# Kernel tuning notes

Hardware: AMD Instinct MI355X
Metric: run time of the kernel (lower is better)

Reference implementation:

```python
import jax, jax.numpy as jnp
import numpy as np

DIM = 1024
STEPS = 4
LEAK = 0.9
RESET = 0.0
EPS = 1e-6


def setup_inputs() -> dict:
    key = jax.random.key(0)
    ks = jax.random.split(key, 5)
    sc = 1.0 / np.sqrt(DIM)
    return {
        "x": jax.random.normal(ks[0], (4, 4096, DIM), dtype=jnp.float32),
        "W_in": jax.random.normal(ks[1], (DIM, DIM), dtype=jnp.float32) * sc,
        "W_inh": jax.random.normal(ks[2], (DIM, DIM), dtype=jnp.float32) * sc,
        "W_out": jax.random.normal(ks[3], (DIM, DIM), dtype=jnp.float32) * sc,
        "threshold_vec": jnp.full((DIM,), 0.5, dtype=jnp.float32),
        "norm_weight": jnp.ones((DIM,), dtype=jnp.float32),
    }


def _rmsnorm(y, w):
    # RMSNorm: y * rsqrt(mean(y^2)) * w
    ms = jnp.mean(y * y, axis=-1, keepdims=True)
    return y * jax.lax.rsqrt(ms + EPS) * w


def reference(x, W_in, W_inh, W_out, threshold_vec, norm_weight):
    # x: [B, L, D]
    membrane = jnp.zeros_like(x)
    current = x @ W_in.T  # same every step; computed once (identical math)
    spike_sum = jnp.zeros_like(x)
    prev_spike = None
    for step in range(STEPS):
        membrane = membrane + current
        if step > 0:
            membrane = membrane - 0.1 * (prev_spike @ W_inh.T)
        fire_mask = (membrane > threshold_vec).astype(x.dtype)
        fire_soft = jax.nn.sigmoid((membrane - threshold_vec) * 10.0)
        # straight-through estimator: hard mask fwd, sigmoid grad
        fire_mask_grad = fire_mask - jax.lax.stop_gradient(fire_soft) + fire_soft
        spike = fire_mask_grad * membrane
        spike_sum = spike_sum + spike
        prev_spike = spike
        membrane = (membrane * (1.0 - fire_mask) + RESET * fire_mask) * LEAK
    spike_total = spike_sum / float(STEPS)
    lif_out = spike_total @ W_out.T
    fired_any = (jnp.abs(spike_total) > 1e-6).astype(x.dtype)
    y = x * (1.0 - 0.5 * fired_any) + 0.5 * lif_out
    x_lif = _rmsnorm(y, norm_weight)
    return x_lif, spike_total, membrane
```

## Files before the change

### kernel.cpp

```cpp
#include <hip/hip_runtime.h>
#include <cmath>

#define N_ROWS 16384
#define DIM 1024
#define MARGIN 5e-5
#define MAX_EVENTS 4194304
#define BATCH 8


__global__ __launch_bounds__(64) void zero_cnt(int* cnt) {
  if (threadIdx.x == 0 && blockIdx.x == 0) cnt[0] = 0;
}

__device__ inline void record_event(int* cnt, int* ev, int r, int s, int c) {
  int idx = atomicAdd(cnt, 1);
  if (idx < MAX_EVENTS) ev[idx] = (r << 12) | (s << 10) | c;
}

template<typename TA, int STEP, bool WRITE_SPK>
__global__ __launch_bounds__(256) void gemm_lif(
    const TA* __restrict__ A, const float* __restrict__ B,
    double* __restrict__ cur, double* __restrict__ mem,
    double* __restrict__ spk_out, float* __restrict__ ssum,
    const float* __restrict__ thr, int* cnt, int* ev)
{
  __shared__ double As[16][130];
  __shared__ double Bs[16][130];
  const int tid  = threadIdx.x;
  const int tx   = tid & 15;
  const int ty   = tid >> 4;
  const int col0 = blockIdx.x * 128;
  const int row0 = blockIdx.y * 128;

  const int ar  = tid >> 1;
  const int akc = (tid & 1) * 8;

  double acc[8][8] = {};

  for (int k0 = 0; k0 < DIM; k0 += 16) {
    const TA* ap = &A[(size_t)(row0 + ar) * DIM + (size_t)(k0 + akc)];
#pragma unroll
    for (int u = 0; u < 8; ++u) As[akc + u][ar] = (double)ap[u];
    const float* bp = &B[(size_t)(col0 + ar) * DIM + (size_t)(k0 + akc)];
#pragma unroll
    for (int u = 0; u < 8; ++u) Bs[akc + u][ar] = (double)bp[u];
    __syncthreads();
#pragma unroll
    for (int kk = 0; kk < 16; ++kk) {
      double a[8], b[8];
#pragma unroll
      for (int u = 0; u < 4; ++u) {
        const double2 av = *reinterpret_cast<const double2*>(&As[kk][ty * 8 + 2 * u]);
        a[2 * u] = av.x; a[2 * u + 1] = av.y;
        const double2 bv = *reinterpret_cast<const double2*>(&Bs[kk][tx * 2 + 32 * u]);
        b[2 * u] = bv.x; b[2 * u + 1] = bv.y;
      }
#pragma unroll
      for (int i = 0; i < 8; ++i)
#pragma unroll
        for (int j = 0; j < 8; ++j)
          acc[i][j] = fma(a[i], b[j], acc[i][j]);
    }
    __syncthreads();
  }

#pragma unroll
  for (int i = 0; i < 8; ++i)
#pragma unroll
    for (int j = 0; j < 8; ++j) {
      const int r = row0 + ty * 8 + i;
      const int c = col0 + tx * 2 + (j & 1) + (j >> 1) * 32;
      const size_t e = (size_t)r * DIM + c;
      double m;
      if (STEP == 0) {
        m = acc[i][j];
        cur[e] = m;
      } else {
        const double m1 = __dadd_rn(mem[e], cur[e]);
        const double t2 = __dmul_rn(0.1, acc[i][j]);
        m = __dsub_rn(m1, t2);
      }
      const double t = (double)thr[c];
      if (fabs(m - t) < MARGIN) record_event(cnt, ev, r, STEP, c);
      const bool fire = m > t;
      const double s = fire ? m : 0.0;
      if (WRITE_SPK) spk_out[e] = s;
      if (STEP == 0) ssum[e] = (float)s;
      else           ssum[e] += (float)s;
      mem[e] = fire ? 0.0 : __dmul_rn(m, 0.9);
    }
}

__global__ __launch_bounds__(256) void init_mid(
    const double* __restrict__ mem, const float* __restrict__ ssum,
    float* __restrict__ memlo, float* __restrict__ memhi,
    float* __restrict__ out1)
{
  size_t base = (size_t)blockIdx.x * 2048 + threadIdx.x;
#pragma unroll
  for (int v = 0; v < 8; ++v) {
    size_t e = base + (size_t)v * 256;
    float f = (float)mem[e];
    memlo[e] = f;
    memhi[e] = f;
    out1[e]  = __fmul_rn(ssum[e], 0.25f);
  }
}

__device__ inline void atomicMinF(float* p, float v) {
  unsigned* u = (unsigned*)p;
  unsigned old = __float_as_uint(*p);
  while (__uint_as_float(old) > v) {
    unsigned assumed = old;
    old = atomicCAS(u, assumed, __float_as_uint(v));
    if (old == assumed) break;
  }
}
__device__ inline void atomicMaxF(float* p, float v) {
  unsigned* u = (unsigned*)p;
  unsigned old = __float_as_uint(*p);
  while (__uint_as_float(old) < v) {
    unsigned assumed = old;
    old = atomicCAS(u, assumed, __float_as_uint(v));
    if (old == assumed) break;
  }
}

__global__ __launch_bounds__(256) void transpose_w(
    const float* __restrict__ W, float* __restrict__ Wt)
{
  __shared__ float t[32][33];
  const int bx = blockIdx.x & 31, by = blockIdx.x >> 5;
  const int x = threadIdx.x & 31, y0 = (threadIdx.x >> 5) << 2;
#pragma unroll
  for (int u = 0; u < 4; ++u)
    t[y0 + u][x] = W[(size_t)(by * 32 + y0 + u) * DIM + bx * 32 + x];
  __syncthreads();
#pragma unroll
  for (int u = 0; u < 4; ++u)
    Wt[(size_t)(bx * 32 + y0 + u) * DIM + by * 32 + x] = t[x][y0 + u];
}

__global__ __launch_bounds__(1024) void phase2f(
    const double* __restrict__ cur, const float* __restrict__ Wt,
    const float* __restrict__ thr, const int* __restrict__ cnt,
    const int* __restrict__ ev, float* __restrict__ memlo,
    float* __restrict__ memhi)
{
  __shared__ float spk2[4][DIM][2];
  int total = cnt[0];
  if (total > MAX_EVENTS) total = MAX_EVENTS;
  const int j = threadIdx.x;
  const double tv = (double)thr[j];

  for (int base = blockIdx.x * BATCH; base < total;
       base += gridDim.x * BATCH) {
    const int nb = min(BATCH, total - base);
    int code[BATCH];
#pragma unroll
    for (int v = 0; v < BATCH; ++v) code[v] = ev[base + min(v, nb - 1)];

    double memr[BATCH];

    __syncthreads();
#pragma unroll
    for (int v = 0; v < BATCH; ++v) {
      const int r = code[v] >> 12;
      const double m = cur[(size_t)r * DIM + j];
      bool fire = m > tv;
      if (((code[v] >> 10) & 3) == 0 && j == (code[v] & 1023)) fire = !fire;
      spk2[v >> 1][j][v & 1] = (float)(fire ? m : 0.0);
      memr[v] = fire ? 0.0 : __dmul_rn(m, 0.9);
    }
    __syncthreads();

    for (int s = 1; s < 4; ++s) {
      double acc[BATCH] = {};
      float wa[8];
#pragma unroll
      for (int u = 0; u < 8; ++u) wa[u] = Wt[(size_t)u * DIM + j];
      for (int e0 = 0; e0 < DIM; e0 += 8) {
        float wb[8];
        const int en = (e0 + 8 < DIM) ? (e0 + 8) : 0;
#pragma unroll
        for (int u = 0; u < 8; ++u) wb[u] = Wt[(size_t)(en + u) * DIM + j];
#pragma unroll
        for (int u = 0; u < 8; ++u) {
          const int e = e0 + u;
          const double wd = (double)wa[u];
          const float2 p0 = *reinterpret_cast<const float2*>(&spk2[0][e][0]);
          const float2 p1 = *reinterpret_cast<const float2*>(&spk2[1][e][0]);
          const float2 p2 = *reinterpret_cast<const float2*>(&spk2[2][e][0]);
          const float2 p3 = *reinterpret_cast<const float2*>(&spk2[3][e][0]);
          acc[0] = fma((double)p0.x, wd, acc[0]);
          acc[1] = fma((double)p0.y, wd, acc[1]);
          acc[2] = fma((double)p1.x, wd, acc[2]);
          acc[3] = fma((double)p1.y, wd, acc[3]);
          acc[4] = fma((double)p2.x, wd, acc[4]);
          acc[5] = fma((double)p2.y, wd, acc[5]);
          acc[6] = fma((double)p3.x, wd, acc[6]);
          acc[7] = fma((double)p3.y, wd, acc[7]);
        }
#pragma unroll
        for (int u = 0; u < 8; ++u) wa[u] = wb[u];
      }
      __syncthreads();
#pragma unroll
      for (int v = 0; v < BATCH; ++v) {
        const int r = code[v] >> 12;
        const double m1 = __dadd_rn(memr[v], cur[(size_t)r * DIM + j]);
        const double t2 = __dmul_rn(0.1, acc[v]);
        const double m  = __dsub_rn(m1, t2);
        bool fire = m > tv;
        if (((code[v] >> 10) & 3) == s && j == (code[v] & 1023)) fire = !fire;
        spk2[v >> 1][j][v & 1] = (float)(fire ? m : 0.0);
        memr[v] = fire ? 0.0 : __dmul_rn(m, 0.9);
      }
      __syncthreads();
    }

    for (int v = 0; v < nb; ++v) {
      const int r = code[v] >> 12;
      const float f = (float)memr[v];
      const size_t g = (size_t)r * DIM + j;
      atomicMinF(&memlo[g], f);
      atomicMaxF(&memhi[g], f);
    }
  }
}

__global__ __launch_bounds__(256) void finalize2(
    const float* __restrict__ memlo, const float* __restrict__ memhi,
    float* __restrict__ out2)
{
  size_t base = (size_t)blockIdx.x * 2048 + threadIdx.x;
#pragma unroll
  for (int v = 0; v < 8; ++v) {
    size_t e = base + (size_t)v * 256;
    out2[e] = __fmul_rn(__fadd_rn(memlo[e], memhi[e]), 0.5f);
  }
}

__global__ __launch_bounds__(256) void gemm_wout_epi(
    const float* __restrict__ Asp, const float* __restrict__ B,
    const float* __restrict__ x, float* __restrict__ y, int K)
{
  __shared__ float As[64][17];
  __shared__ float Bs[64][17];
  const int tid  = threadIdx.x;
  const int tx   = tid & 15;
  const int ty   = tid >> 4;
  const int col0 = blockIdx.x * 64;
  const int row0 = blockIdx.y * 64;
  const int lr   = tid >> 2;
  const int lc   = (tid & 3) << 2;

  float acc[4][4] = {};

  for (int k0 = 0; k0 < K; k0 += 16) {
#pragma unroll
    for (int u = 0; u < 4; ++u) {
      As[lr][lc + u] = Asp[(size_t)(row0 + lr) * K + (size_t)(k0 + lc + u)];
      Bs[lr][lc + u] = B[(size_t)(col0 + lr) * K + (size_t)(k0 + lc + u)];
    }
    __syncthreads();
#pragma unroll
    for (int kk = 0; kk < 16; ++kk) {
      float a[4], b[4];
#pragma unroll
      for (int i = 0; i < 4; ++i) a[i] = As[ty * 4 + i][kk];
#pragma unroll
      for (int j = 0; j < 4; ++j) b[j] = Bs[tx * 4 + j][kk];
#pragma unroll
      for (int i = 0; i < 4; ++i)
#pragma unroll
        for (int j = 0; j < 4; ++j)
          acc[i][j] = fmaf(a[i], b[j], acc[i][j]);
    }
    __syncthreads();
  }

#pragma unroll
  for (int i = 0; i < 4; ++i)
#pragma unroll
    for (int j = 0; j < 4; ++j) {
      size_t idx = (size_t)(row0 + ty * 4 + i) * DIM + (size_t)(col0 + tx * 4 + j);
      float st    = Asp[idx] * 0.25f;
      float fired = (fabsf(st) > 1e-6f) ? 1.0f : 0.0f;
      float lif   = 0.25f * acc[i][j];
      y[idx] = x[idx] * (1.0f - 0.5f * fired) + 0.5f * lif;
    }
}

__global__ __launch_bounds__(256) void rmsnorm_k(
    const float* __restrict__ y, const float* __restrict__ wn,
    float* __restrict__ out)
{
  const int row = blockIdx.x;
  const int tid = threadIdx.x;
  const float4 v = reinterpret_cast<const float4*>(y + (size_t)row * DIM)[tid];
  double ss = (double)v.x * v.x + (double)v.y * v.y +
              (double)v.z * v.z + (double)v.w * v.w;
#pragma unroll
  for (int off = 32; off; off >>= 1) ss += __shfl_down(ss, off, 64);
  __shared__ double warr[4];
  if ((tid & 63) == 0) warr[tid >> 6] = ss;
  __syncthreads();
  double tot = warr[0] + warr[1] + warr[2] + warr[3];
  float r = rsqrtf((float)(tot * (1.0 / 1024.0)) + 1e-6f);
  const float4 wv = reinterpret_cast<const float4*>(wn)[tid];
  float4 o;
  o.x = v.x * r * wv.x;
  o.y = v.y * r * wv.y;
  o.z = v.z * r * wv.z;
  o.w = v.w * r * wv.w;
  reinterpret_cast<float4*>(out + (size_t)row * DIM)[tid] = o;
}

extern "C" void kernel_launch(void* const* d_in, const int* in_sizes, int n_in,
                              void* d_out, int out_size, void* d_ws, size_t ws_size,
                              hipStream_t stream) {
  const float* x     = (const float*)d_in[0];
  const float* W_in  = (const float*)d_in[1];
  const float* W_inh = (const float*)d_in[2];
  const float* W_out = (const float*)d_in[3];
  const float* thr   = (const float*)d_in[4];
  const float* nw    = (const float*)d_in[5];

  const size_t nd = (size_t)N_ROWS * DIM;
  float* out0 = (float*)d_out;
  float* out1 = out0 + nd;
  float* out2 = out1 + nd;

  char* p = (char*)d_ws;
  double* cur  = (double*)p; p += nd * sizeof(double);
  double* mem  = (double*)p; p += nd * sizeof(double);
  double* spk0 = (double*)p; p += nd * sizeof(double);
  double* spk1 = (double*)p; p += nd * sizeof(double);
  float*  ssum = (float*)p;  p += nd * sizeof(float);

  float* memlo = (float*)spk0;
  float* memhi = (float*)spk0 + nd;
  float* ybuf  = (float*)spk1;
  float* Wt    = out0;
  int* evcnt = (int*)out2;
  int* ev    = (int*)out2 + 4;

  dim3 ggrid3(DIM / 128, N_ROWS / 128);
  dim3 ggrid(DIM / 64, N_ROWS / 64);
  const int egrid = (int)(nd / 2048);

  zero_cnt<<<1, 64, 0, stream>>>(evcnt);
  transpose_w<<<1024, 256, 0, stream>>>(W_inh, Wt);
  gemm_lif<float, 0, true><<<ggrid3, 256, 0, stream>>>(
      x, W_in, cur, mem, spk0, ssum, thr, evcnt, ev);
  gemm_lif<double, 1, true><<<ggrid3, 256, 0, stream>>>(
      spk0, W_inh, cur, mem, spk1, ssum, thr, evcnt, ev);
  gemm_lif<double, 2, true><<<ggrid3, 256, 0, stream>>>(
      spk1, W_inh, cur, mem, spk0, ssum, thr, evcnt, ev);
  gemm_lif<double, 3, false><<<ggrid3, 256, 0, stream>>>(
      spk0, W_inh, cur, mem, spk1, ssum, thr, evcnt, ev);
  init_mid<<<egrid, 256, 0, stream>>>(mem, ssum, memlo, memhi, out1);
  phase2f<<<2048, 1024, 0, stream>>>(cur, Wt, thr, evcnt, ev, memlo, memhi);
  finalize2<<<egrid, 256, 0, stream>>>(memlo, memhi, out2);
  gemm_wout_epi<<<ggrid, 256, 0, stream>>>(ssum, W_out, x, ybuf, DIM);
  rmsnorm_k<<<N_ROWS, 256, 0, stream>>>(ybuf, nw, out0);
}
```

Baseline: 4.913 ms.

## Split near-threshold event handling per step with incremental rank-one fork updates

Near-threshold events now go into one queue per step and record the hard fire decision. Each queue gets its own handler instead of replaying all steps from step 0. Step-3 events only flip the final reset, and step-2 events apply a rank-one W_inh correction to the stored float membrane. Step-0 and step-1 events start from the saved intermediate membranes, so they simulate fewer full matvec steps. In exchange the kernel stores float intermediate membranes, launches more kernels and caps each queue at a fixed size, which could drop events.

New measurement: 4.490 ms. 8.6% less time.

```diff
diff --git a/kernel.cpp b/kernel.cpp
--- a/kernel.cpp
+++ b/kernel.cpp
@@ -4,17 +4,17 @@
 #define N_ROWS 16384
 #define DIM 1024
 #define MARGIN 5e-5
-#define MAX_EVENTS 4194304
+#define CAP 32768
 #define BATCH 8
 
 
-__global__ __launch_bounds__(64) void zero_cnt(int* cnt) {
-  if (threadIdx.x == 0 && blockIdx.x == 0) cnt[0] = 0;
-}
-
-__device__ inline void record_event(int* cnt, int* ev, int r, int s, int c) {
+__global__ void zero_cnts(int* cnt) {
+  if (blockIdx.x == 0 && threadIdx.x < 4) cnt[threadIdx.x] = 0;
+}
+
+__device__ inline void record_event(int* cnt, int* evq, int r, int c, bool fire) {
   int idx = atomicAdd(cnt, 1);
-  if (idx < MAX_EVENTS) ev[idx] = (r << 12) | (s << 10) | c;
+  if (idx < CAP) evq[idx] = (r << 11) | (fire ? 1024 : 0) | c;
 }
 
 template<typename TA, int STEP, bool WRITE_SPK>
@@ -22,7 +22,8 @@
     const TA* __restrict__ A, const float* __restrict__ B,
     double* __restrict__ cur, double* __restrict__ mem,
     double* __restrict__ spk_out, float* __restrict__ ssum,
-    const float* __restrict__ thr, int* cnt, int* ev)
+    float* __restrict__ mf, const float* __restrict__ thr,
+    int* cnt, int* evq)
 {
   __shared__ double As[16][130];
   __shared__ double Bs[16][130];
@@ -81,29 +82,41 @@
         m = __dsub_rn(m1, t2);
       }
       const double t = (double)thr[c];
-      if (fabs(m - t) < MARGIN) record_event(cnt, ev, r, STEP, c);
       const bool fire = m > t;
+      if (fabs(m - t) < MARGIN) record_event(cnt, evq, r, c, fire);
       const double s = fire ? m : 0.0;
       if (WRITE_SPK) spk_out[e] = s;
       if (STEP == 0) ssum[e] = (float)s;
       else           ssum[e] += (float)s;
-      mem[e] = fire ? 0.0 : __dmul_rn(m, 0.9);
-    }
-}
-
-__global__ __launch_bounds__(256) void init_mid(
-    const double* __restrict__ mem, const float* __restrict__ ssum,
-    float* __restrict__ memlo, float* __restrict__ memhi,
-    float* __restrict__ out1)
+      if (STEP > 0)  mf[e] = (float)m;
+      if (STEP < 3)  mem[e] = fire ? 0.0 : __dmul_rn(m, 0.9);
+    }
+}
+
+__global__ __launch_bounds__(256) void init_hull(
+    const float* __restrict__ m3f, const float* __restrict__ thr,
+    float* __restrict__ memlo, float* __restrict__ memhi)
 {
   size_t base = (size_t)blockIdx.x * 2048 + threadIdx.x;
 #pragma unroll
   for (int v = 0; v < 8; ++v) {
     size_t e = base + (size_t)v * 256;
-    float f = (float)mem[e];
-    memlo[e] = f;
-    memhi[e] = f;
-    out1[e]  = __fmul_rn(ssum[e], 0.25f);
+    const double m = (double)m3f[e];
+    const bool fire = m > (double)thr[e & 1023];
+    const float val = fire ? 0.0f : (float)__dmul_rn(m, 0.9);
+    memlo[e] = val;
+    memhi[e] = val;
+  }
+}
+
+__global__ __launch_bounds__(256) void write_out1(
+    const float* __restrict__ ssum, float* __restrict__ out1)
+{
+  size_t base = (size_t)blockIdx.x * 2048 + threadIdx.x;
+#pragma unroll
+  for (int v = 0; v < 8; ++v) {
+    size_t e = base + (size_t)v * 256;
+    out1[e] = __fmul_rn(ssum[e], 0.25f);
   }
 }
 
@@ -141,15 +154,64 @@
     Wt[(size_t)(bx * 32 + y0 + u) * DIM + by * 32 + x] = t[x][y0 + u];
 }
 
-__global__ __launch_bounds__(1024) void phase2f(
-    const double* __restrict__ cur, const float* __restrict__ Wt,
+__global__ __launch_bounds__(256) void fork3(
+    const float* __restrict__ m3f, const int* __restrict__ cnt,
+    const int* __restrict__ evq, float* __restrict__ memlo,
+    float* __restrict__ memhi)
+{
+  int total = min(cnt[3], CAP);
+  for (int i = blockIdx.x * 256 + threadIdx.x; i < total;
+       i += gridDim.x * 256) {
+    const int code = evq[i];
+    const int r = code >> 11;
+    const bool fireA = (code >> 10) & 1;
+    const int c = code & 1023;
+    const size_t g = (size_t)r * DIM + c;
+    const double m = (double)m3f[g];
+    const float val = fireA ? (float)__dmul_rn(m, 0.9) : 0.0f;
+    atomicMinF(&memlo[g], val);
+    atomicMaxF(&memhi[g], val);
+  }
+}
+
+__global__ __launch_bounds__(256) void fork2(
+    const float* __restrict__ m2f, const float* __restrict__ m3f,
+    const float* __restrict__ Wt, const float* __restrict__ thr,
+    const int* __restrict__ cnt, const int* __restrict__ evq,
+    float* __restrict__ memlo, float* __restrict__ memhi)
+{
+  int total = min(cnt[2], CAP);
+  for (int i = blockIdx.x; i < total; i += gridDim.x) {
+    const int code = evq[i];
+    const int r = code >> 11;
+    const bool fireA = (code >> 10) & 1;
+    const int eF = code & 1023;
+    const double mS  = (double)m2f[(size_t)r * DIM + eF];
+    const double Dlt = fireA ? -mS : mS;
+#pragma unroll
+    for (int q = 0; q < 4; ++q) {
+      const int j = threadIdx.x + q * 256;
+      const size_t g = (size_t)r * DIM + j;
+      double mB = (double)m3f[g] - 0.1 * Dlt * (double)Wt[(size_t)eF * DIM + j];
+      if (j == eF) mB -= 0.9 * Dlt;
+      const bool fire = mB > (double)thr[j];
+      const float val = fire ? 0.0f : (float)(mB * 0.9);
+      atomicMinF(&memlo[g], val);
+      atomicMaxF(&memhi[g], val);
+    }
+  }
+}
+
+template<int SF>
+__global__ __launch_bounds__(1024) void fork01(
+    const double* __restrict__ cur, const float* __restrict__ m1f,
+    const float* __restrict__ m2f, const float* __restrict__ Wt,
     const float* __restrict__ thr, const int* __restrict__ cnt,
-    const int* __restrict__ ev, float* __restrict__ memlo,
+    const int* __restrict__ evq, float* __restrict__ memlo,
     float* __restrict__ memhi)
 {
   __shared__ float spk2[4][DIM][2];
-  int total = cnt[0];
-  if (total > MAX_EVENTS) total = MAX_EVENTS;
+  int total = min(cnt[SF], CAP);
   const int j = threadIdx.x;
   const double tv = (double)thr[j];
 
@@ -158,23 +220,30 @@
     const int nb = min(BATCH, total - base);
     int code[BATCH];
 #pragma unroll
-    for (int v = 0; v < BATCH; ++v) code[v] = ev[base + min(v, nb - 1)];
+    for (int v = 0; v < BATCH; ++v) code[v] = evq[base + min(v, nb - 1)];
 
     double memr[BATCH];
 
     __syncthreads();
 #pragma unroll
     for (int v = 0; v < BATCH; ++v) {
-      const int r = code[v] >> 12;
-      const double m = cur[(size_t)r * DIM + j];
-      bool fire = m > tv;
-      if (((code[v] >> 10) & 3) == 0 && j == (code[v] & 1023)) fire = !fire;
-      spk2[v >> 1][j][v & 1] = (float)(fire ? m : 0.0);
-      memr[v] = fire ? 0.0 : __dmul_rn(m, 0.9);
-    }
-    __syncthreads();
-
-    for (int s = 1; s < 4; ++s) {
+      const int r = code[v] >> 11;
+      const bool fireA = (code[v] >> 10) & 1;
+      const int eF = code[v] & 1023;
+      const double mS = (SF == 0) ? cur[(size_t)r * DIM + eF]
+                                  : (double)m1f[(size_t)r * DIM + eF];
+      const double Dlt = fireA ? -mS : mS;
+      const float* basef = (SF == 0) ? m1f : m2f;
+      double mB = (double)basef[(size_t)r * DIM + j]
+                  - 0.1 * Dlt * (double)Wt[(size_t)eF * DIM + j];
+      if (j == eF) mB -= 0.9 * Dlt;
+      const bool fire = mB > tv;
+      spk2[v >> 1][j][v & 1] = (float)(fire ? mB : 0.0);
+      memr[v] = fire ? 0.0 : __dmul_rn(mB, 0.9);
+    }
+    __syncthreads();
+
+    for (int t = SF + 2; t < 4; ++t) {
       double acc[BATCH] = {};
       float wa[8];
 #pragma unroll
@@ -207,12 +276,10 @@
       __syncthreads();
 #pragma unroll
       for (int v = 0; v < BATCH; ++v) {
-        const int r = code[v] >> 12;
-        const double m1 = __dadd_rn(memr[v], cur[(size_t)r * DIM + j]);
-        const double t2 = __dmul_rn(0.1, acc[v]);
-        const double m  = __dsub_rn(m1, t2);
-        bool fire = m > tv;
-        if (((code[v] >> 10) & 3) == s && j == (code[v] & 1023)) fire = !fire;
+        const int r = code[v] >> 11;
+        const double m1_ = __dadd_rn(memr[v], cur[(size_t)r * DIM + j]);
+        const double m   = __dsub_rn(m1_, __dmul_rn(0.1, acc[v]));
+        const bool fire = m > tv;
         spk2[v >> 1][j][v & 1] = (float)(fire ? m : 0.0);
         memr[v] = fire ? 0.0 : __dmul_rn(m, 0.9);
       }
@@ -220,7 +287,7 @@
     }
 
     for (int v = 0; v < nb; ++v) {
-      const int r = code[v] >> 12;
+      const int r = code[v] >> 11;
       const float f = (float)memr[v];
       const size_t g = (size_t)r * DIM + j;
       atomicMinF(&memlo[g], f);
@@ -339,30 +406,41 @@
   double* spk1 = (double*)p; p += nd * sizeof(double);
   float*  ssum = (float*)p;  p += nd * sizeof(float);
 
+  float* Wt    = out0;
+  int*   evb   = (int*)(out0 + (1 << 20));
+  int*   evcnt = evb;
+  int*   evq0  = evb + 16;
+  float* m1f   = out1;
+  float* m2f   = out2;
+  float* m3f   = (float*)spk1 + nd;
   float* memlo = (float*)spk0;
   float* memhi = (float*)spk0 + nd;
   float* ybuf  = (float*)spk1;
-  float* Wt    = out0;
-  int* evcnt = (int*)out2;
-  int* ev    = (int*)out2 + 4;
 
   dim3 ggrid3(DIM / 128, N_ROWS / 128);
   dim3 ggrid(DIM / 64, N_ROWS / 64);
   const int egrid = (int)(nd / 2048);
 
-  zero_cnt<<<1, 64, 0, stream>>>(evcnt);
+  zero_cnts<<<1, 64, 0, stream>>>(evcnt);
   transpose_w<<<1024, 256, 0, stream>>>(W_inh, Wt);
   gemm_lif<float, 0, true><<<ggrid3, 256, 0, stream>>>(
-      x, W_in, cur, mem, spk0, ssum, thr, evcnt, ev);
+      x, W_in, cur, mem, spk0, ssum, nullptr, thr, evcnt + 0, evq0 + 0 * CAP);
   gemm_lif<double, 1, true><<<ggrid3, 256, 0, stream>>>(
-      spk0, W_inh, cur, mem, spk1, ssum, thr, evcnt, ev);
+      spk0, W_inh, cur, mem, spk1, ssum, m1f, thr, evcnt + 1, evq0 + 1 * CAP);
   gemm_lif<double, 2, true><<<ggrid3, 256, 0, stream>>>(
-      spk1, W_inh, cur, mem, spk0, ssum, thr, evcnt, ev);
+      spk1, W_inh, cur, mem, spk0, ssum, m2f, thr, evcnt + 2, evq0 + 2 * CAP);
   gemm_lif<double, 3, false><<<ggrid3, 256, 0, stream>>>(
-      spk0, W_inh, cur, mem, spk1, ssum, thr, evcnt, ev);
-  init_mid<<<egrid, 256, 0, stream>>>(mem, ssum, memlo, memhi, out1);
-  phase2f<<<2048, 1024, 0, stream>>>(cur, Wt, thr, evcnt, ev, memlo, memhi);
+      spk0, W_inh, cur, mem, nullptr, ssum, m3f, thr, evcnt + 3, evq0 + 3 * CAP);
+  init_hull<<<egrid, 256, 0, stream>>>(m3f, thr, memlo, memhi);
+  fork3<<<64, 256, 0, stream>>>(m3f, evcnt, evq0 + 3 * CAP, memlo, memhi);
+  fork2<<<2048, 256, 0, stream>>>(m2f, m3f, Wt, thr, evcnt, evq0 + 2 * CAP,
+                                  memlo, memhi);
+  fork01<1><<<512, 1024, 0, stream>>>(cur, m1f, m2f, Wt, thr, evcnt,
+                                      evq0 + 1 * CAP, memlo, memhi);
+  fork01<0><<<512, 1024, 0, stream>>>(cur, m1f, m2f, Wt, thr, evcnt,
+                                      evq0 + 0 * CAP, memlo, memhi);
   finalize2<<<egrid, 256, 0, stream>>>(memlo, memhi, out2);
+  write_out1<<<egrid, 256, 0, stream>>>(ssum, out1);
   gemm_wout_epi<<<ggrid, 256, 0, stream>>>(ssum, W_out, x, ybuf, DIM);
   rmsnorm_k<<<N_ROWS, 256, 0, stream>>>(ybuf, nw, out0);
 }
```
